# Kernel optimization log

Hardware: AMD Instinct MI355X
Metric: run time of the kernel (lower is better)

The kernel has to match this reference:

```python
import jax, jax.numpy as jnp
import numpy as np

N = 131072  # total sentences
D = 768     # relation/sentence embedding dim
B = 16384   # number of bags (scopes)
C = 53      # n_class (NYT10 relations)


def setup_inputs() -> dict:
    key = jax.random.key(0)
    k1, k2, k3, k4, k5 = jax.random.split(key, 5)
    x = jax.random.normal(k1, (N, D), dtype=jnp.float32)
    label = jax.random.randint(k2, (N,), 0, C)              # per-sentence bag label
    segment_ids = jnp.sort(jax.random.randint(k3, (N,), 0, B))  # sorted -> contiguous scopes
    rel_weight = jax.random.normal(k4, (C, D), dtype=jnp.float32) * 0.05  # relation_matrix.weight
    bias = jax.random.normal(k5, (C,), dtype=jnp.float32)
    return {"x": x, "label": label, "segment_ids": segment_ids,
            "rel_weight": rel_weight, "bias": bias}


def reference(x, label, segment_ids, rel_weight, bias):
    # _attention_train_logit: <x_i, relation_matrix[label_i]>  -> [N]
    att = jnp.sum(x * rel_weight[label], axis=1)
    # per-bag (segment) stable softmax over sentences in each scope
    seg_max = jax.ops.segment_max(att, segment_ids, num_segments=B)      # [B]
    e = jnp.exp(att - seg_max[segment_ids])                              # [N]
    denom = jax.ops.segment_sum(e, segment_ids, num_segments=B)         # [B]
    # softmax-weighted pooling: sum_i softmax_i * x_i per bag
    num = jax.ops.segment_sum(e[:, None] * x, segment_ids, num_segments=B)  # [B, D]
    repre = num / jnp.where(denom == 0, 1.0, denom)[:, None]
    # get_logits (dropout=0.0 -> identity)
    logits = repre @ rel_weight.T + bias                                 # [B, C]
    return logits
```

## Files before the change

kernel.cpp:

```cpp
#include <hip/hip_runtime.h>
#include <math.h>

#define DN   768
#define NC   53
#define NCP  64
#define NKC  6
#define MBLK 64

typedef __attribute__((ext_vector_type(8))) __bf16 bf16x8;
typedef __attribute__((ext_vector_type(8))) short short8v;
typedef __attribute__((ext_vector_type(4))) float f32x4;

static __device__ __forceinline__ unsigned short f2bf(float f) {
    unsigned int u = __builtin_bit_cast(unsigned int, f);
    u = (u + 0x7FFFu + ((u >> 16) & 1u)) >> 16;
    return (unsigned short)u;
}
static __device__ __forceinline__ float bf2f(unsigned short h) {
    unsigned int u = ((unsigned int)h) << 16;
    return __builtin_bit_cast(float, u);
}

#define GLOAD16(gptr, lptr)                                        \
    __builtin_amdgcn_global_load_lds(                              \
        (const __attribute__((address_space(1))) void*)(gptr),     \
        (__attribute__((address_space(3))) void*)(lptr), 16, 0, 0)

__global__ void prep_kernel(const float* __restrict__ w,
                            const int*   __restrict__ seg,
                            unsigned short* __restrict__ wb,
                            int* __restrict__ offs,
                            int N, int B) {
    const int bid = blockIdx.x;
    if (bid < 192) {
        int i = bid * 256 + threadIdx.x;
        const int e    = i & 7;
        const int lane = (i >> 3) & 63;
        const int ct   = (i >> 9) & 3;
        const int ks   = i >> 11;
        const int cls  = ct * 16 + (lane & 15);
        const int k    = ks * 32 + ((lane >> 4) << 3) + e;
        wb[i] = (cls < NC) ? f2bf(w[cls * DN + k]) : (unsigned short)0;
    } else {
        int i = (bid - 192) * 256 + threadIdx.x;
        if (i >= N) return;
        int cur  = seg[i];
        int prev = (i == 0) ? -1 : seg[i - 1];
        for (int b = prev + 1; b <= cur; ++b) offs[b] = i;
        if (i == N - 1)
            for (int b = cur + 1; b <= B; ++b) offs[b] = N;
    }
}

__global__ __launch_bounds__(256) void gemm_y5(
    const float* __restrict__ x,
    const int*   __restrict__ label,
    const unsigned short* __restrict__ wb,
    unsigned short* __restrict__ yb,
    float* __restrict__ att)
{
    __shared__ float          xs[2][4][16][128];
    __shared__ unsigned short yt[4][16][66];

    const int lane = threadIdx.x & 63;
    const int wv   = threadIdx.x >> 6;
    const int r16  = lane & 15;
    const int kg   = lane >> 4;
    const long row0w = (long)blockIdx.x * MBLK + wv * 16;

    f32x4 acc[4];
    #pragma unroll
    for (int ct = 0; ct < 4; ++ct) acc[ct] = (f32x4){0.f, 0.f, 0.f, 0.f};

    const int srowp = lane >> 5;
    const int sgs   = lane & 31;
    char* const xsb = (char*)xs;

    short8v lb[2][4][4];

#define ISSUE_LB(buf, ch)                                                      \
    {                                                                          \
        _Pragma("unroll")                                                      \
        for (int ks = 0; ks < 4; ++ks)                                         \
            _Pragma("unroll")                                                  \
            for (int ct = 0; ct < 4; ++ct)                                     \
                lb[buf][ks][ct] = *(const short8v*)(                           \
                    wb + ((((ch) * 4 + ks) * 4 + ct) * 64 + lane) * 8);        \
    }

#define STAGE(buf, ch)                                                         \
    {                                                                          \
        _Pragma("unroll")                                                      \
        for (int i = 0; i < 8; ++i) {                                          \
            const int rl = 2 * i + srowp;                                      \
            const int gx = sgs ^ (rl & 7);         \
            const float* sp = x + (row0w + rl) * (long)DN + (ch) * 128 + gx * 4;\
            char* lp = xsb + (buf) * 32768 + wv * 8192 + i * 1024; \
            GLOAD16(sp, lp);                                                   \
        }                                                                      \
    }

    ISSUE_LB(0, 0)
    STAGE(0, 0)

    #pragma unroll
    for (int ch = 0; ch < NKC; ++ch) {
        const int cur = ch & 1, nxt = cur ^ 1;
        if (ch + 1 < NKC) {
            ISSUE_LB(nxt, ch + 1)
            STAGE(nxt, ch + 1)
            asm volatile("s_waitcnt vmcnt(24)" ::: "memory");
        } else {
            asm volatile("s_waitcnt vmcnt(0)" ::: "memory");
        }
        #pragma unroll
        for (int ks = 0; ks < 4; ++ks) {
            const char* base = xsb + cur * 32768 + wv * 8192 + r16 * 512;
            const int g0 = ks * 8 + kg * 2;
            const float4 u0 = *(const float4*)(base + ((g0    ) ^ (r16 & 7)) * 16);
            const float4 u1 = *(const float4*)(base + ((g0 + 1) ^ (r16 & 7)) * 16);
            bf16x8 a8;
            a8[0] = (__bf16)u0.x; a8[1] = (__bf16)u0.y;
            a8[2] = (__bf16)u0.z; a8[3] = (__bf16)u0.w;
            a8[4] = (__bf16)u1.x; a8[5] = (__bf16)u1.y;
            a8[6] = (__bf16)u1.z; a8[7] = (__bf16)u1.w;
            #pragma unroll
            for (int ct = 0; ct < 4; ++ct)
                acc[ct] = __builtin_amdgcn_mfma_f32_16x16x32_bf16(
                    a8, __builtin_bit_cast(bf16x8, lb[cur][ks][ct]), acc[ct], 0, 0, 0);
        }
    }

#undef ISSUE_LB
#undef STAGE

    #pragma unroll
    for (int ct = 0; ct < 4; ++ct)
        #pragma unroll
        for (int r = 0; r < 4; ++r) {
            const int   rl = kg * 4 + r;
            const float v  = acc[ct][r];
            yb[(row0w + rl) * NCP + ct * 16 + r16] = f2bf(v);
            yt[wv][rl][ct * 16 + r16] = f2bf(v);
        }
    if (lane < 16) {
        const long grow = row0w + lane;
        const int  lab  = label[grow];
        att[grow] = bf2f(yt[wv][lane][lab]);
    }
}

__global__ __launch_bounds__(256) void pool_kernel(
    const unsigned short* __restrict__ yb,
    const float* __restrict__ att,
    const int*   __restrict__ offs,
    const float* __restrict__ bias,
    float*       __restrict__ out,
    int Btot)
{
    __shared__ float s_e[4][64];
    const int wv   = threadIdx.x >> 6;
    const int lane = threadIdx.x & 63;
    const int bag  = blockIdx.x * 4 + wv;
    if (bag >= Btot) return;
    const int s = offs[bag], e = offs[bag + 1];

    float m = -INFINITY, den = 0.f, facc = 0.f;
    for (int j0 = s; j0 < e; j0 += 64) {
        const int j = j0 + lane;
        float a = (j < e) ? att[j] : -INFINITY;
        float cm = a;
        #pragma unroll
        for (int off = 1; off < 64; off <<= 1) cm = fmaxf(cm, __shfl_xor(cm, off));
        const float nm = fmaxf(m, cm);
        const float sc = __expf(m - nm);
        const float ej = (j < e) ? __expf(a - nm) : 0.f;
        float cd = ej;
        #pragma unroll
        for (int off = 1; off < 64; off <<= 1) cd += __shfl_xor(cd, off);
        den = den * sc + cd;
        s_e[wv][lane] = ej;
        const int cnt = min(64, e - j0);
        float f0 = 0.f, f1 = 0.f, f2 = 0.f, f3 = 0.f;
        int t = 0;
        for (; t + 4 <= cnt; t += 4) {
            f0 += s_e[wv][t]     * bf2f(yb[(size_t)(j0 + t)     * NCP + lane]);
            f1 += s_e[wv][t + 1] * bf2f(yb[(size_t)(j0 + t + 1) * NCP + lane]);
            f2 += s_e[wv][t + 2] * bf2f(yb[(size_t)(j0 + t + 2) * NCP + lane]);
            f3 += s_e[wv][t + 3] * bf2f(yb[(size_t)(j0 + t + 3) * NCP + lane]);
        }
        for (; t < cnt; ++t)
            f0 += s_e[wv][t] * bf2f(yb[(size_t)(j0 + t) * NCP + lane]);
        facc = facc * sc + ((f0 + f1) + (f2 + f3));
        m = nm;
    }
    if (lane < NC) {
        const float inv = (den == 0.f) ? 0.f : 1.f / den;
        out[(size_t)bag * NC + lane] = facc * inv + bias[lane];
    }
}

extern "C" void kernel_launch(void* const* d_in, const int* in_sizes, int n_in,
                              void* d_out, int out_size, void* d_ws, size_t ws_size,
                              hipStream_t stream)
{
    const float* x     = (const float*)d_in[0];
    const int*   label = (const int*)  d_in[1];
    const int*   seg   = (const int*)  d_in[2];
    const float* w     = (const float*)d_in[3];
    const float* bias  = (const float*)d_in[4];
    float*       out   = (float*)d_out;

    const int N = in_sizes[0] / DN;
    const int B = out_size / NC;

    unsigned short* wb   = (unsigned short*)d_ws;
    int*            offs = (int*)((char*)d_ws + 131072);
    float*          att  = (float*)((char*)d_ws + 1048576);
    unsigned short* yb   = (unsigned short*)((char*)d_ws + 2097152);

    hipLaunchKernelGGL(prep_kernel, dim3(192 + (N + 255) / 256), dim3(256), 0, stream,
                       w, seg, wb, offs, N, B);
    hipLaunchKernelGGL(gemm_y5, dim3(N / MBLK), dim3(256), 0, stream,
                       x, label, wb, yb, att);
    hipLaunchKernelGGL(pool_kernel, dim3((B + 3) / 4), dim3(256), 0, stream,
                       yb, att, offs, bias, out, B);
}
```

Before: 110.4 us.

## Triple-buffer smaller K chunks in GEMM and extract attention via shuffles

The GEMM now splits K into 12 chunks of 64 instead of 6 chunks of 128. x is staged into a triple-buffered LDS ring that prefetches two chunks ahead, with vmcnt waits retuned to match, and the weight register double-buffer is shrunk accordingly. Launch bounds request 3 blocks per CU, and the smaller LDS footprint makes that possible. The per-row attention value is now pulled from the accumulators with lane shuffles instead of a bf16 LDS staging tile, which drops an LDS buffer and keeps att in full fp32. The aim is more memory-latency hiding on the streaming read of x, at the cost of more loop iterations and waits.

```diff
diff --git a/kernel.cpp b/kernel.cpp
--- a/kernel.cpp
+++ b/kernel.cpp
@@ -4,7 +4,8 @@
 #define DN   768
 #define NC   53
 #define NCP  64
-#define NKC  6
+#define KC   64
+#define NKC  12
 #define MBLK 64
 
 typedef __attribute__((ext_vector_type(8))) __bf16 bf16x8;
@@ -37,9 +38,9 @@
         const int e    = i & 7;
         const int lane = (i >> 3) & 63;
         const int ct   = (i >> 9) & 3;
-        const int ks   = i >> 11;
+        const int kk   = i >> 11;
         const int cls  = ct * 16 + (lane & 15);
-        const int k    = ks * 32 + ((lane >> 4) << 3) + e;
+        const int k    = kk * 32 + ((lane >> 4) << 3) + e;
         wb[i] = (cls < NC) ? f2bf(w[cls * DN + k]) : (unsigned short)0;
     } else {
         int i = (bid - 192) * 256 + threadIdx.x;
@@ -52,73 +53,73 @@
     }
 }
 
-__global__ __launch_bounds__(256) void gemm_y5(
+__global__ __launch_bounds__(256, 3) void gemm_y6(
     const float* __restrict__ x,
     const int*   __restrict__ label,
     const unsigned short* __restrict__ wb,
     unsigned short* __restrict__ yb,
     float* __restrict__ att)
 {
-    __shared__ float          xs[2][4][16][128];
-    __shared__ unsigned short yt[4][16][66];
+    __shared__ float xs[3][4][16][KC];
 
     const int lane = threadIdx.x & 63;
     const int wv   = threadIdx.x >> 6;
     const int r16  = lane & 15;
     const int kg   = lane >> 4;
     const long row0w = (long)blockIdx.x * MBLK + wv * 16;
+    char* const xsb = (char*)xs;
 
     f32x4 acc[4];
     #pragma unroll
     for (int ct = 0; ct < 4; ++ct) acc[ct] = (f32x4){0.f, 0.f, 0.f, 0.f};
 
-    const int srowp = lane >> 5;
-    const int sgs   = lane & 31;
-    char* const xsb = (char*)xs;
-
-    short8v lb[2][4][4];
-
-#define ISSUE_LB(buf, ch)                                                      \
+    const int srl = lane >> 4;
+    const int sgs = lane & 15;
+    short8v lb[2][2][4];
+
+#define ISSUE_LB(par, ch)                                                      \
     {                                                                          \
         _Pragma("unroll")                                                      \
-        for (int ks = 0; ks < 4; ++ks)                                         \
+        for (int ks = 0; ks < 2; ++ks)                                         \
             _Pragma("unroll")                                                  \
             for (int ct = 0; ct < 4; ++ct)                                     \
-                lb[buf][ks][ct] = *(const short8v*)(                           \
-                    wb + ((((ch) * 4 + ks) * 4 + ct) * 64 + lane) * 8);        \
+                lb[par][ks][ct] = *(const short8v*)(                           \
+                    wb + ((((ch) * 2 + ks) * 4 + ct) * 64 + lane) * 8);        \
     }
 
 #define STAGE(buf, ch)                                                         \
     {                                                                          \
         _Pragma("unroll")                                                      \
-        for (int i = 0; i < 8; ++i) {                                          \
-            const int rl = 2 * i + srowp;                                      \
-            const int gx = sgs ^ (rl & 7);         \
-            const float* sp = x + (row0w + rl) * (long)DN + (ch) * 128 + gx * 4;\
-            char* lp = xsb + (buf) * 32768 + wv * 8192 + i * 1024; \
+        for (int i = 0; i < 4; ++i) {                                          \
+            const int rl = i * 4 + srl;                                        \
+            const int g  = sgs ^ (rl & 7);         \
+            const float* sp = x + (row0w + rl) * (long)DN + (ch) * KC + g * 4; \
+            char* lp = xsb + (buf) * 16384 + wv * 4096 + i * 1024;             \
             GLOAD16(sp, lp);                                                   \
         }                                                                      \
     }
 
+    STAGE(0, 0)
     ISSUE_LB(0, 0)
-    STAGE(0, 0)
+    STAGE(1, 1)
 
     #pragma unroll
     for (int ch = 0; ch < NKC; ++ch) {
-        const int cur = ch & 1, nxt = cur ^ 1;
-        if (ch + 1 < NKC) {
-            ISSUE_LB(nxt, ch + 1)
-            STAGE(nxt, ch + 1)
-            asm volatile("s_waitcnt vmcnt(24)" ::: "memory");
-        } else {
-            asm volatile("s_waitcnt vmcnt(0)" ::: "memory");
-        }
-        #pragma unroll
-        for (int ks = 0; ks < 4; ++ks) {
-            const char* base = xsb + cur * 32768 + wv * 8192 + r16 * 512;
+        const int cur = ch % 3;
+        const int lpar = ch & 1;
+        if (ch + 1 < NKC) ISSUE_LB(lpar ^ 1, ch + 1)
+        if (ch + 2 < NKC) STAGE((ch + 2) % 3, ch + 2)
+        if (ch <= NKC - 3)      asm volatile("s_waitcnt vmcnt(16)" ::: "memory");
+        else if (ch == NKC - 2) asm volatile("s_waitcnt vmcnt(12)" ::: "memory");
+        else                    asm volatile("s_waitcnt vmcnt(0)"  ::: "memory");
+
+        const char* abase = xsb + cur * 16384 + wv * 4096 + r16 * 256;
+        const int sw = r16 & 7;
+        #pragma unroll
+        for (int ks = 0; ks < 2; ++ks) {
             const int g0 = ks * 8 + kg * 2;
-            const float4 u0 = *(const float4*)(base + ((g0    ) ^ (r16 & 7)) * 16);
-            const float4 u1 = *(const float4*)(base + ((g0 + 1) ^ (r16 & 7)) * 16);
+            const float4 u0 = *(const float4*)(abase + ((g0    ) ^ sw) * 16);
+            const float4 u1 = *(const float4*)(abase + ((g0 + 1) ^ sw) * 16);
             bf16x8 a8;
             a8[0] = (__bf16)u0.x; a8[1] = (__bf16)u0.y;
             a8[2] = (__bf16)u0.z; a8[3] = (__bf16)u0.w;
@@ -127,7 +128,7 @@
             #pragma unroll
             for (int ct = 0; ct < 4; ++ct)
                 acc[ct] = __builtin_amdgcn_mfma_f32_16x16x32_bf16(
-                    a8, __builtin_bit_cast(bf16x8, lb[cur][ks][ct]), acc[ct], 0, 0, 0);
+                    a8, __builtin_bit_cast(bf16x8, lb[lpar][ks][ct]), acc[ct], 0, 0, 0);
         }
     }
 
@@ -137,17 +138,20 @@
     #pragma unroll
     for (int ct = 0; ct < 4; ++ct)
         #pragma unroll
+        for (int r = 0; r < 4; ++r)
+            yb[(row0w + kg * 4 + r) * NCP + ct * 16 + r16] = f2bf(acc[ct][r]);
+
+    const int lab = (lane < 16) ? label[row0w + lane] : 0;
+    const int srcl = ((lane >> 2) << 4) | (lab & 15);
+    float av = 0.f;
+    #pragma unroll
+    for (int ct = 0; ct < 4; ++ct)
+        #pragma unroll
         for (int r = 0; r < 4; ++r) {
-            const int   rl = kg * 4 + r;
-            const float v  = acc[ct][r];
-            yb[(row0w + rl) * NCP + ct * 16 + r16] = f2bf(v);
-            yt[wv][rl][ct * 16 + r16] = f2bf(v);
+            const float v = __shfl(acc[ct][r], srcl);
+            if ((lab >> 4) == ct && (lane & 3) == r) av = v;
         }
-    if (lane < 16) {
-        const long grow = row0w + lane;
-        const int  lab  = label[grow];
-        att[grow] = bf2f(yt[wv][lane][lab]);
-    }
+    if (lane < 16) att[row0w + lane] = av;
 }
 
 __global__ __launch_bounds__(256) void pool_kernel(
@@ -221,7 +225,7 @@
 
     hipLaunchKernelGGL(prep_kernel, dim3(192 + (N + 255) / 256), dim3(256), 0, stream,
                        w, seg, wb, offs, N, B);
-    hipLaunchKernelGGL(gemm_y5, dim3(N / MBLK), dim3(256), 0, stream,
+    hipLaunchKernelGGL(gemm_y6, dim3(N / MBLK), dim3(256), 0, stream,
                        x, label, wb, yb, att);
     hipLaunchKernelGGL(pool_kernel, dim3((B + 3) / 4), dim3(256), 0, stream,
                        yb, att, offs, bias, out, B);
```

Result: slower. 113.0 us (+2.3%).

## Fuse softmax-weighted pooling into GEMM epilogue with atomic per-bag accumulation

Applied to the files above, without the earlier changes.

The GEMM epilogue now computes exp(att) for each row and accumulates exp-weighted logit rows and the denominator per bag with global atomics into a zeroed buffer. This removes the separate pooling kernel, the bf16 intermediate Y and att writes, and the segment-offset computation. A small final kernel then divides by the denominator and adds the bias. The softmax no longer subtracts the per-bag max, so it relies on attention values staying small enough not to overflow exp. Float atomics also make the summation order nondeterministic.

```diff
diff --git a/kernel.cpp b/kernel.cpp
--- a/kernel.cpp
+++ b/kernel.cpp
@@ -27,46 +27,43 @@
         (__attribute__((address_space(3))) void*)(lptr), 16, 0, 0)
 
 __global__ void prep_kernel(const float* __restrict__ w,
-                            const int*   __restrict__ seg,
                             unsigned short* __restrict__ wb,
-                            int* __restrict__ offs,
-                            int N, int B) {
+                            float* __restrict__ num,
+                            int Btot) {
     const int bid = blockIdx.x;
     if (bid < 192) {
         int i = bid * 256 + threadIdx.x;
         const int e    = i & 7;
         const int lane = (i >> 3) & 63;
         const int ct   = (i >> 9) & 3;
-        const int ks   = i >> 11;
+        const int kk   = i >> 11;
         const int cls  = ct * 16 + (lane & 15);
-        const int k    = ks * 32 + ((lane >> 4) << 3) + e;
+        const int k    = kk * 32 + ((lane >> 4) << 3) + e;
         wb[i] = (cls < NC) ? f2bf(w[cls * DN + k]) : (unsigned short)0;
     } else {
         int i = (bid - 192) * 256 + threadIdx.x;
-        if (i >= N) return;
-        int cur  = seg[i];
-        int prev = (i == 0) ? -1 : seg[i - 1];
-        for (int b = prev + 1; b <= cur; ++b) offs[b] = i;
-        if (i == N - 1)
-            for (int b = cur + 1; b <= B; ++b) offs[b] = N;
-    }
-}
-
-__global__ __launch_bounds__(256) void gemm_y5(
+        if (i < Btot * 65) num[i] = 0.f;
+    }
+}
+
+__global__ __launch_bounds__(256) void gemm_fused(
     const float* __restrict__ x,
     const int*   __restrict__ label,
+    const int*   __restrict__ seg,
     const unsigned short* __restrict__ wb,
-    unsigned short* __restrict__ yb,
-    float* __restrict__ att)
+    float* __restrict__ num)
 {
     __shared__ float          xs[2][4][16][128];
     __shared__ unsigned short yt[4][16][66];
+    __shared__ float          se[4][16];
+    __shared__ int            sg[4][16];
 
     const int lane = threadIdx.x & 63;
     const int wv   = threadIdx.x >> 6;
     const int r16  = lane & 15;
     const int kg   = lane >> 4;
     const long row0w = (long)blockIdx.x * MBLK + wv * 16;
+    char* const xsb = (char*)xs;
 
     f32x4 acc[4];
     #pragma unroll
@@ -74,8 +71,6 @@
 
     const int srowp = lane >> 5;
     const int sgs   = lane & 31;
-    char* const xsb = (char*)xs;
-
     short8v lb[2][4][4];
 
 #define ISSUE_LB(buf, ch)                                                      \
@@ -117,8 +112,9 @@
         for (int ks = 0; ks < 4; ++ks) {
             const char* base = xsb + cur * 32768 + wv * 8192 + r16 * 512;
             const int g0 = ks * 8 + kg * 2;
-            const float4 u0 = *(const float4*)(base + ((g0    ) ^ (r16 & 7)) * 16);
-            const float4 u1 = *(const float4*)(base + ((g0 + 1) ^ (r16 & 7)) * 16);
+            const int sw = r16 & 7;
+            const float4 u0 = *(const float4*)(base + ((g0    ) ^ sw) * 16);
+            const float4 u1 = *(const float4*)(base + ((g0 + 1) ^ sw) * 16);
             bf16x8 a8;
             a8[0] = (__bf16)u0.x; a8[1] = (__bf16)u0.y;
             a8[2] = (__bf16)u0.z; a8[3] = (__bf16)u0.w;
@@ -137,66 +133,45 @@
     #pragma unroll
     for (int ct = 0; ct < 4; ++ct)
         #pragma unroll
-        for (int r = 0; r < 4; ++r) {
-            const int   rl = kg * 4 + r;
-            const float v  = acc[ct][r];
-            yb[(row0w + rl) * NCP + ct * 16 + r16] = f2bf(v);
-            yt[wv][rl][ct * 16 + r16] = f2bf(v);
-        }
+        for (int r = 0; r < 4; ++r)
+            yt[wv][kg * 4 + r][ct * 16 + r16] = f2bf(acc[ct][r]);
+    asm volatile("s_waitcnt lgkmcnt(0)" ::: "memory");
+
     if (lane < 16) {
         const long grow = row0w + lane;
-        const int  lab  = label[grow];
-        att[grow] = bf2f(yt[wv][lane][lab]);
-    }
-}
-
-__global__ __launch_bounds__(256) void pool_kernel(
-    const unsigned short* __restrict__ yb,
-    const float* __restrict__ att,
-    const int*   __restrict__ offs,
+        sg[wv][lane] = seg[grow];
+        se[wv][lane] = __expf(bf2f(yt[wv][lane][label[grow]]));
+    }
+    asm volatile("s_waitcnt lgkmcnt(0)" ::: "memory");
+
+    float a = 0.f, d = 0.f;
+    #pragma unroll
+    for (int r = 0; r < 16; ++r) {
+        const float e = se[wv][r];
+        a = fmaf(e, bf2f(yt[wv][r][lane]), a);
+        d += e;
+        if (r == 15 || sg[wv][r + 1] != sg[wv][r]) {
+            float* np = num + (long)sg[wv][r] * 65;
+            atomicAdd(np + lane, a);
+            if (lane == 0) atomicAdd(np + 64, d);
+            a = 0.f; d = 0.f;
+        }
+    }
+}
+
+__global__ __launch_bounds__(256) void final_kernel(
+    const float* __restrict__ num,
     const float* __restrict__ bias,
     float*       __restrict__ out,
     int Btot)
 {
-    __shared__ float s_e[4][64];
-    const int wv   = threadIdx.x >> 6;
-    const int lane = threadIdx.x & 63;
-    const int bag  = blockIdx.x * 4 + wv;
-    if (bag >= Btot) return;
-    const int s = offs[bag], e = offs[bag + 1];
-
-    float m = -INFINITY, den = 0.f, facc = 0.f;
-    for (int j0 = s; j0 < e; j0 += 64) {
-        const int j = j0 + lane;
-        float a = (j < e) ? att[j] : -INFINITY;
-        float cm = a;
-        #pragma unroll
-        for (int off = 1; off < 64; off <<= 1) cm = fmaxf(cm, __shfl_xor(cm, off));
-        const float nm = fmaxf(m, cm);
-        const float sc = __expf(m - nm);
-        const float ej = (j < e) ? __expf(a - nm) : 0.f;
-        float cd = ej;
-        #pragma unroll
-        for (int off = 1; off < 64; off <<= 1) cd += __shfl_xor(cd, off);
-        den = den * sc + cd;
-        s_e[wv][lane] = ej;
-        const int cnt = min(64, e - j0);
-        float f0 = 0.f, f1 = 0.f, f2 = 0.f, f3 = 0.f;
-        int t = 0;
-        for (; t + 4 <= cnt; t += 4) {
-            f0 += s_e[wv][t]     * bf2f(yb[(size_t)(j0 + t)     * NCP + lane]);
-            f1 += s_e[wv][t + 1] * bf2f(yb[(size_t)(j0 + t + 1) * NCP + lane]);
-            f2 += s_e[wv][t + 2] * bf2f(yb[(size_t)(j0 + t + 2) * NCP + lane]);
-            f3 += s_e[wv][t + 3] * bf2f(yb[(size_t)(j0 + t + 3) * NCP + lane]);
-        }
-        for (; t < cnt; ++t)
-            f0 += s_e[wv][t] * bf2f(yb[(size_t)(j0 + t) * NCP + lane]);
-        facc = facc * sc + ((f0 + f1) + (f2 + f3));
-        m = nm;
-    }
-    if (lane < NC) {
+    const int i = blockIdx.x * 256 + threadIdx.x;
+    if (i >= Btot * 64) return;
+    const int bag = i >> 6, c = i & 63;
+    if (c < NC) {
+        const float den = num[(long)bag * 65 + 64];
         const float inv = (den == 0.f) ? 0.f : 1.f / den;
-        out[(size_t)bag * NC + lane] = facc * inv + bias[lane];
+        out[(long)bag * NC + c] = num[(long)bag * 65 + c] * inv + bias[c];
     }
 }
 
@@ -214,15 +189,14 @@
     const int N = in_sizes[0] / DN;
     const int B = out_size / NC;
 
-    unsigned short* wb   = (unsigned short*)d_ws;
-    int*            offs = (int*)((char*)d_ws + 131072);
-    float*          att  = (float*)((char*)d_ws + 1048576);
-    unsigned short* yb   = (unsigned short*)((char*)d_ws + 2097152);
-
-    hipLaunchKernelGGL(prep_kernel, dim3(192 + (N + 255) / 256), dim3(256), 0, stream,
-                       w, seg, wb, offs, N, B);
-    hipLaunchKernelGGL(gemm_y5, dim3(N / MBLK), dim3(256), 0, stream,
-                       x, label, wb, yb, att);
-    hipLaunchKernelGGL(pool_kernel, dim3((B + 3) / 4), dim3(256), 0, stream,
-                       yb, att, offs, bias, out, B);
-}
+    unsigned short* wb  = (unsigned short*)d_ws;
+    float*          num = (float*)((char*)d_ws + 1048576);
+
+    const int zblocks = (B * 65 + 255) / 256;
+    hipLaunchKernelGGL(prep_kernel, dim3(192 + zblocks), dim3(256), 0, stream,
+                       w, wb, num, B);
+    hipLaunchKernelGGL(gemm_fused, dim3(N / MBLK), dim3(256), 0, stream,
+                       x, label, seg, wb, num);
+    hipLaunchKernelGGL(final_kernel, dim3((B * 64 + 255) / 256), dim3(256), 0, stream,
+                       num, bias, out, B);
+}
```

Result: faster. 104.3 us (-5.6%).
